# Kernel optimization log

Hardware: AMD Instinct MI355X
Metric: run time of the kernel (lower is better)

Reference implementation:

```python
import jax, jax.numpy as jnp
import numpy as np

TAU_PRE = 2.0   # pre-synaptic trace time constant
SCALE = 1.0     # forward(scale=1.0) default
SPIKE_P = 0.1   # firing probability for realistic binary spike trains


def setup_inputs() -> dict:
    key = jax.random.key(0)
    k1, k2 = jax.random.split(key)
    T, B, NIN, NOUT = 2048, 128, 256, 128
    # binary spike trains, [T, B, N]
    in_spikes = (jax.random.uniform(k1, (T, B, NIN)) < SPIKE_P).astype(jnp.float32)
    out_spikes = (jax.random.uniform(k2, (T, B, NOUT)) < SPIKE_P).astype(jnp.float32)
    return {"in_spikes": in_spikes, "out_spikes": out_spikes}


def reference(in_spikes, out_spikes):
    # STDP.forward: loop over recorded timesteps, per step:
    #   trace_pre = trace_pre - trace_pre/tau_pre + in_spike          (decayed trace)
    #   dw = sum_b trace_pre[b, :] (outer) out_spike[b, :] -> [NOUT, NIN]
    #   delta_w += scale * dw
    # Expressed as a single lax.scan over the time axis.
    B, NIN = in_spikes.shape[1], in_spikes.shape[2]
    NOUT = out_spikes.shape[2]

    def step(carry, xs):
        trace_pre, delta_w = carry
        s_in, s_out = xs                                 # [B, NIN], [B, NOUT]
        trace_pre = trace_pre - trace_pre / TAU_PRE + s_in
        dw = jnp.einsum('bi,bo->oi', trace_pre, s_out)   # [NOUT, NIN]
        return (trace_pre, delta_w + SCALE * dw), None

    init = (jnp.zeros((B, NIN), in_spikes.dtype),
            jnp.zeros((NOUT, NIN), in_spikes.dtype))
    (_, delta_w), _ = jax.lax.scan(step, init, (in_spikes, out_spikes))
    return delta_w
```

## Files before the change

### kernel.cpp

```cpp
#include <hip/hip_runtime.h>
#include <hip/hip_bf16.h>

#define T_TOTAL 2048
#define BATCH   128
#define NIN     256
#define NOUT    128

#define TC      256
#define BC      4
#define WARM    32
#define G       4
#define NTC     (T_TOTAL / TC)
#define NBC     (BATCH / BC)
#define NBLOCKS (NTC * NBC)
#define NG      (TC / G)

#define OUT_ELEMS (NOUT * NIN)

static_assert(NG % 2 == 0, "2-stage pipeline needs even group count");

typedef __attribute__((ext_vector_type(8)))  __bf16 bf16x8;
typedef __attribute__((ext_vector_type(2)))  __bf16 bf16x2;
typedef __attribute__((ext_vector_type(16))) float  f32x16;

static __device__ __forceinline__ unsigned pack_bf16(float a, float b) {
    bf16x2 v = { (__bf16)a, (__bf16)b };
    union { bf16x2 v; unsigned u; } c; c.v = v; return c.u;
}

static __device__ __forceinline__ bf16x8 frag_from4(unsigned d0, unsigned d1,
                                                    unsigned d2, unsigned d3) {
    union { unsigned u[4]; bf16x8 v; } c;
    c.u[0] = d0; c.u[1] = d1; c.u[2] = d2; c.u[3] = d3; return c.v;
}

__global__ __launch_bounds__(512, 2)
void stdp_main(const float* __restrict__ in, const float* __restrict__ outs,
               float* __restrict__ dst, int nslots, int use_atomic)
{
    const int tid = threadIdx.x;
    const int bc  = blockIdx.x % NBC;
    const int tc  = blockIdx.x / NBC;
    const int b0  = bc * BC;
    const int t0  = tc * TC;

    const int lane = tid & 63;
    const int wv   = tid >> 6;
    const int mt   = wv & 3;
    const int nh   = wv >> 2;
    const int l31  = lane & 31;
    const int kh   = lane >> 5;

    const size_t IST = (size_t)BATCH * NIN;
    const size_t OST = (size_t)BATCH * NOUT;

    const float* __restrict__ inW  = in   + (size_t)(b0 + 2 * kh) * NIN  + nh * 128 + l31;
    const float* __restrict__ outW = outs + (size_t)(b0 + 2 * kh) * NOUT + mt * 32  + l31;

    float rtrA = 0.f, rtrB = 0.f;

    if (tc < NTC - 1) {
        for (int tb = t0 + TC + WARM; tb > t0 + TC; tb -= 8) {
            float vA[8], vB[8];
#pragma unroll
            for (int u = 0; u < 8; ++u) {
                vA[u] = outW[(size_t)(tb - 1 - u) * OST];
                vB[u] = outW[(size_t)(tb - 1 - u) * OST + NOUT];
            }
#pragma unroll
            for (int u = 0; u < 8; ++u) {
                rtrA = vA[u] + 0.5f * rtrA;
                rtrB = vB[u] + 0.5f * rtrB;
            }
        }
    }

    f32x16 acc[4];
#pragma unroll
    for (int j = 0; j < 4; ++j) acc[j] = (f32x16)(0.f);

    float AO[2][8];
    float BI[2][32];

    auto load_stage = [&](int s, int g) {
        const int tg = t0 + g * G;
#pragma unroll
        for (int q = 0; q < G; ++q) {
            AO[s][q]     = outW[(size_t)(tg + q) * OST];
            AO[s][4 + q] = outW[(size_t)(tg + q) * OST + NOUT];
        }
#pragma unroll
        for (int tn = 0; tn < 4; ++tn)
#pragma unroll
            for (int be = 0; be < 2; ++be)
#pragma unroll
                for (int q = 0; q < G; ++q)
                    BI[s][tn * 8 + be * 4 + q] =
                        inW[(size_t)(tg + q) * IST + be * NIN + tn * 32];
    };

    auto body = [&](int s, int g) {
        float aA[4], aB[4];
#pragma unroll
        for (int q = 3; q >= 0; --q) {
            rtrA = AO[s][q]     + 0.5f * rtrA; aA[q] = rtrA;
            rtrB = AO[s][4 + q] + 0.5f * rtrB; aB[q] = rtrB;
        }
        const bf16x8 a = frag_from4(pack_bf16(aA[0], aA[1]), pack_bf16(aA[2], aA[3]),
                                    pack_bf16(aB[0], aB[1]), pack_bf16(aB[2], aB[3]));
        bf16x8 bfr[4];
#pragma unroll
        for (int tn = 0; tn < 4; ++tn) {
            const float* p = &BI[s][tn * 8];
            bfr[tn] = frag_from4(pack_bf16(p[0], p[1]), pack_bf16(p[2], p[3]),
                                 pack_bf16(p[4], p[5]), pack_bf16(p[6], p[7]));
        }
        if (g >= 2) load_stage(s, g - 2);
#pragma unroll
        for (int tn = 0; tn < 4; ++tn)
            acc[tn] = __builtin_amdgcn_mfma_f32_32x32x16_bf16(a, bfr[tn], acc[tn], 0, 0, 0);
    };

    load_stage(1, NG - 1);
    load_stage(0, NG - 2);
    for (int gg = NG - 1; gg >= 1; gg -= 2) {
        body(1, gg);
        body(0, gg - 1);
    }

    float* base = dst + (size_t)(use_atomic ? (blockIdx.x % nslots) : blockIdx.x) * OUT_ELEMS;
#pragma unroll
    for (int j = 0; j < 4; ++j) {
        const int icol = (nh * 4 + j) * 32 + l31;
#pragma unroll
        for (int r = 0; r < 16; ++r) {
            const int row = (r & 3) + 8 * (r >> 2) + 4 * kh;
            const int o   = mt * 32 + row;
            const float v = acc[j][r];
            if (use_atomic) atomicAdd(&base[o * NIN + icol], v);
            else            base[o * NIN + icol] = v;
        }
    }
}

__global__ void zero_kernel(float* p, int n) {
    int i = blockIdx.x * blockDim.x + threadIdx.x;
    if (i < n) p[i] = 0.f;
}

__global__ __launch_bounds__(256)
void reduce_kernel(const float* __restrict__ ws, float* __restrict__ outp, int nslots) {
    const int idx = blockIdx.x * 256 + threadIdx.x;
    float s = 0.f;
    int k = 0;
    for (; k + 16 <= nslots; k += 16) {
        float v[16];
#pragma unroll
        for (int u = 0; u < 16; ++u) v[u] = ws[(size_t)(k + u) * OUT_ELEMS + idx];
#pragma unroll
        for (int u = 0; u < 16; ++u) s += v[u];
    }
    for (; k < nslots; ++k) s += ws[(size_t)k * OUT_ELEMS + idx];
    outp[idx] = s;
}

extern "C" void kernel_launch(void* const* d_in, const int* in_sizes, int n_in,
                              void* d_out, int out_size, void* d_ws, size_t ws_size,
                              hipStream_t stream) {
    const float* in   = (const float*)d_in[0];
    const float* outs = (const float*)d_in[1];
    float* out = (float*)d_out;
    float* ws  = (float*)d_ws;

    const size_t slot_bytes = (size_t)OUT_ELEMS * sizeof(float);

    if (ws_size >= (size_t)NBLOCKS * slot_bytes) {
        stdp_main<<<NBLOCKS, 512, 0, stream>>>(in, outs, ws, NBLOCKS, 0);
        reduce_kernel<<<OUT_ELEMS / 256, 256, 0, stream>>>(ws, out, NBLOCKS);
    } else if (ws_size >= 16 * slot_bytes) {
        zero_kernel<<<(16 * OUT_ELEMS + 255) / 256, 256, 0, stream>>>(ws, 16 * OUT_ELEMS);
        stdp_main<<<NBLOCKS, 512, 0, stream>>>(in, outs, ws, 16, 1);
        reduce_kernel<<<OUT_ELEMS / 256, 256, 0, stream>>>(ws, out, 16);
    } else {
        zero_kernel<<<(OUT_ELEMS + 255) / 256, 256, 0, stream>>>(out, OUT_ELEMS);
        stdp_main<<<NBLOCKS, 512, 0, stream>>>(in, outs, out, 1, 1);
    }
}
```

Measured before the change: 453.8 us.

## Replace workspace slot reduction with direct atomics into output, rotating write order

Removes the per-block workspace slots and the separate reduce kernel. Every block now atomically adds its partial delta_w tile straight into the zeroed output. The atomic order is rotated by block index so that concurrent blocks hit different addresses and contend less. This saves the workspace write/read round trip and one launch, but adds heavy atomic contention: 256 blocks each add into the same 32K floats.

Result: slower. 476.1 us (+4.9%).

```diff
diff --git a/kernel.cpp b/kernel.cpp
--- a/kernel.cpp
+++ b/kernel.cpp
@@ -36,7 +36,7 @@
 
 __global__ __launch_bounds__(512, 2)
 void stdp_main(const float* __restrict__ in, const float* __restrict__ outs,
-               float* __restrict__ dst, int nslots, int use_atomic)
+               float* __restrict__ dst)
 {
     const int tid = threadIdx.x;
     const int bc  = blockIdx.x % NBC;
@@ -128,17 +128,18 @@
         body(0, gg - 1);
     }
 
-    float* base = dst + (size_t)(use_atomic ? (blockIdx.x % nslots) : blockIdx.x) * OUT_ELEMS;
+    const int jrot = blockIdx.x & 3;
+    const int rrot = (blockIdx.x >> 2) & 15;
 #pragma unroll
-    for (int j = 0; j < 4; ++j) {
+    for (int jj = 0; jj < 4; ++jj) {
+        const int j    = (jj + jrot) & 3;
         const int icol = (nh * 4 + j) * 32 + l31;
 #pragma unroll
-        for (int r = 0; r < 16; ++r) {
+        for (int rr = 0; rr < 16; ++rr) {
+            const int r   = (rr + rrot) & 15;
             const int row = (r & 3) + 8 * (r >> 2) + 4 * kh;
             const int o   = mt * 32 + row;
-            const float v = acc[j][r];
-            if (use_atomic) atomicAdd(&base[o * NIN + icol], v);
-            else            base[o * NIN + icol] = v;
+            atomicAdd(&dst[o * NIN + icol], acc[j][r]);
         }
     }
 }
@@ -148,41 +149,13 @@
     if (i < n) p[i] = 0.f;
 }
 
-__global__ __launch_bounds__(256)
-void reduce_kernel(const float* __restrict__ ws, float* __restrict__ outp, int nslots) {
-    const int idx = blockIdx.x * 256 + threadIdx.x;
-    float s = 0.f;
-    int k = 0;
-    for (; k + 16 <= nslots; k += 16) {
-        float v[16];
-#pragma unroll
-        for (int u = 0; u < 16; ++u) v[u] = ws[(size_t)(k + u) * OUT_ELEMS + idx];
-#pragma unroll
-        for (int u = 0; u < 16; ++u) s += v[u];
-    }
-    for (; k < nslots; ++k) s += ws[(size_t)k * OUT_ELEMS + idx];
-    outp[idx] = s;
-}
-
 extern "C" void kernel_launch(void* const* d_in, const int* in_sizes, int n_in,
                               void* d_out, int out_size, void* d_ws, size_t ws_size,
                               hipStream_t stream) {
     const float* in   = (const float*)d_in[0];
     const float* outs = (const float*)d_in[1];
     float* out = (float*)d_out;
-    float* ws  = (float*)d_ws;
 
-    const size_t slot_bytes = (size_t)OUT_ELEMS * sizeof(float);
-
-    if (ws_size >= (size_t)NBLOCKS * slot_bytes) {
-        stdp_main<<<NBLOCKS, 512, 0, stream>>>(in, outs, ws, NBLOCKS, 0);
-        reduce_kernel<<<OUT_ELEMS / 256, 256, 0, stream>>>(ws, out, NBLOCKS);
-    } else if (ws_size >= 16 * slot_bytes) {
-        zero_kernel<<<(16 * OUT_ELEMS + 255) / 256, 256, 0, stream>>>(ws, 16 * OUT_ELEMS);
-        stdp_main<<<NBLOCKS, 512, 0, stream>>>(in, outs, ws, 16, 1);
-        reduce_kernel<<<OUT_ELEMS / 256, 256, 0, stream>>>(ws, out, 16);
-    } else {
-        zero_kernel<<<(OUT_ELEMS + 255) / 256, 256, 0, stream>>>(out, OUT_ELEMS);
-        stdp_main<<<NBLOCKS, 512, 0, stream>>>(in, outs, out, 1, 1);
-    }
+    zero_kernel<<<(OUT_ELEMS + 255) / 256, 256, 0, stream>>>(out, OUT_ELEMS);
+    stdp_main<<<NBLOCKS, 512, 0, stream>>>(in, outs, out);
 }
```

## Stage spike tiles through LDS with async global_load_lds double buffering

Applied to the files above, without the earlier changes.

Replaces the per-thread strided scalar global loads of the input and output spike tiles with wide 16-byte global-to-LDS direct loads. The block cooperatively DMAs each group of timesteps into a double-buffered shared-memory tile, then reads MFMA operands from LDS. This is meant to turn many uncoalesced 4-byte global loads into coalesced 16-byte transfers. In exchange it adds 48 KB of LDS per block, two block barriers per group, and explicit vmcnt waits, which may limit occupancy and serialize the pipeline.

Result: faster. 442.8 us (-2.4%).

```diff
diff --git a/kernel.cpp b/kernel.cpp
--- a/kernel.cpp
+++ b/kernel.cpp
@@ -34,10 +34,20 @@
     c.u[0] = d0; c.u[1] = d1; c.u[2] = d2; c.u[3] = d3; return c.v;
 }
 
+static __device__ __forceinline__ void gload16(const float* g, void* l) {
+    __builtin_amdgcn_global_load_lds(
+        (const __attribute__((address_space(1))) void*)g,
+        (__attribute__((address_space(3))) void*)l,
+        16, 0, 0);
+}
+
 __global__ __launch_bounds__(512, 2)
 void stdp_main(const float* __restrict__ in, const float* __restrict__ outs,
                float* __restrict__ dst, int nslots, int use_atomic)
 {
+    __shared__ float in_lds [2][G * BC * NIN];
+    __shared__ float out_lds[2][G * BC * NOUT];
+
     const int tid = threadIdx.x;
     const int bc  = blockIdx.x % NBC;
     const int tc  = blockIdx.x / NBC;
@@ -51,14 +61,10 @@
     const int l31  = lane & 31;
     const int kh   = lane >> 5;
 
-    const size_t IST = (size_t)BATCH * NIN;
     const size_t OST = (size_t)BATCH * NOUT;
 
-    const float* __restrict__ inW  = in   + (size_t)(b0 + 2 * kh) * NIN  + nh * 128 + l31;
-    const float* __restrict__ outW = outs + (size_t)(b0 + 2 * kh) * NOUT + mt * 32  + l31;
-
+    const float* __restrict__ outW = outs + (size_t)(b0 + 2 * kh) * NOUT + mt * 32 + l31;
     float rtrA = 0.f, rtrB = 0.f;
-
     if (tc < NTC - 1) {
         for (int tb = t0 + TC + WARM; tb > t0 + TC; tb -= 8) {
             float vA[8], vB[8];
@@ -79,54 +85,74 @@
 #pragma unroll
     for (int j = 0; j < 4; ++j) acc[j] = (f32x16)(0.f);
 
-    float AO[2][8];
-    float BI[2][32];
-
-    auto load_stage = [&](int s, int g) {
+    const float* inS  = in   + (size_t)(b0 + (wv & 3)) * NIN  + lane * 4;
+    const float* outS = outs + (size_t)(b0 + 2 * (wv & 1) + kh) * NOUT + l31 * 4;
+    const int    tin  = wv >> 2;
+    const int    tot  = wv >> 1;
+    char* inL  = (char*)&in_lds[0][0]  + wv * 1024;
+    char* outL = (char*)&out_lds[0][0] + wv * 1024;
+
+    auto dma_group = [&](int s, int g) {
         const int tg = t0 + g * G;
-#pragma unroll
-        for (int q = 0; q < G; ++q) {
-            AO[s][q]     = outW[(size_t)(tg + q) * OST];
-            AO[s][4 + q] = outW[(size_t)(tg + q) * OST + NOUT];
-        }
-#pragma unroll
-        for (int tn = 0; tn < 4; ++tn)
-#pragma unroll
-            for (int be = 0; be < 2; ++be)
-#pragma unroll
-                for (int q = 0; q < G; ++q)
-                    BI[s][tn * 8 + be * 4 + q] =
-                        inW[(size_t)(tg + q) * IST + be * NIN + tn * 32];
+        gload16(inS  + (size_t)(tg + tin)     * (BATCH * NIN),  inL + s * 16384);
+        gload16(inS  + (size_t)(tg + tin + 2) * (BATCH * NIN),  inL + s * 16384 + 8192);
+        gload16(outS + (size_t)(tg + tot)     * (BATCH * NOUT), outL + s * 8192);
     };
 
-    auto body = [&](int s, int g) {
+    const char* ilb = (const char*)&in_lds [0][0] + kh * 2048 + nh * 512 + l31 * 4;
+    const char* olb = (const char*)&out_lds[0][0] + kh * 1024 + mt * 128 + l31 * 4;
+
+    auto body = [&](int s, int g, int vm) {
+        if (vm) asm volatile("s_waitcnt vmcnt(3)" ::: "memory");
+        else    asm volatile("s_waitcnt vmcnt(0)" ::: "memory");
+        __builtin_amdgcn_s_barrier();
+        __builtin_amdgcn_sched_barrier(0);
+
+        float vA[4], vB[4];
+#pragma unroll
+        for (int q = 0; q < 4; ++q) {
+            vA[q] = *(const float*)(olb + s * 8192 + q * 2048);
+            vB[q] = *(const float*)(olb + s * 8192 + q * 2048 + 512);
+        }
         float aA[4], aB[4];
 #pragma unroll
         for (int q = 3; q >= 0; --q) {
-            rtrA = AO[s][q]     + 0.5f * rtrA; aA[q] = rtrA;
-            rtrB = AO[s][4 + q] + 0.5f * rtrB; aB[q] = rtrB;
+            rtrA = vA[q] + 0.5f * rtrA; aA[q] = rtrA;
+            rtrB = vB[q] + 0.5f * rtrB; aB[q] = rtrB;
         }
         const bf16x8 a = frag_from4(pack_bf16(aA[0], aA[1]), pack_bf16(aA[2], aA[3]),
                                     pack_bf16(aB[0], aB[1]), pack_bf16(aB[2], aB[3]));
         bf16x8 bfr[4];
 #pragma unroll
         for (int tn = 0; tn < 4; ++tn) {
-            const float* p = &BI[s][tn * 8];
+            float p[8];
+#pragma unroll
+            for (int be = 0; be < 2; ++be)
+#pragma unroll
+                for (int q = 0; q < 4; ++q)
+                    p[be * 4 + q] = *(const float*)
+                        (ilb + s * 16384 + q * 4096 + be * 1024 + tn * 128);
             bfr[tn] = frag_from4(pack_bf16(p[0], p[1]), pack_bf16(p[2], p[3]),
                                  pack_bf16(p[4], p[5]), pack_bf16(p[6], p[7]));
         }
-        if (g >= 2) load_stage(s, g - 2);
 #pragma unroll
         for (int tn = 0; tn < 4; ++tn)
             acc[tn] = __builtin_amdgcn_mfma_f32_32x32x16_bf16(a, bfr[tn], acc[tn], 0, 0, 0);
+
+        asm volatile("s_waitcnt lgkmcnt(0)" ::: "memory");
+        __builtin_amdgcn_s_barrier();
+        __builtin_amdgcn_sched_barrier(0);
+        if (g >= 2) dma_group(s, g - 2);
     };
 
-    load_stage(1, NG - 1);
-    load_stage(0, NG - 2);
-    for (int gg = NG - 1; gg >= 1; gg -= 2) {
-        body(1, gg);
-        body(0, gg - 1);
-    }
+    dma_group(1, NG - 1);
+    dma_group(0, NG - 2);
+    for (int gg = NG - 1; gg >= 3; gg -= 2) {
+        body(1, gg, 1);
+        body(0, gg - 1, 1);
+    }
+    body(1, 1, 1);
+    body(0, 0, 0);
 
     float* base = dst + (size_t)(use_atomic ? (blockIdx.x % nslots) : blockIdx.x) * OUT_ELEMS;
 #pragma unroll
```
